# Kernel optimization log

Measured on AMD Instinct MI355X. Metric: run time of the kernel, lower is better.

The kernel has to match this reference:

```python
import jax, jax.numpy as jnp
import numpy as np

EMBED_DIM = 1024
N_HEADS = 16
HEAD_DIM = EMBED_DIM // N_HEADS  # 64
ROPE_DIM = 4
N_FREQ = HEAD_DIM // (2 * ROPE_DIM)  # 8 rotary freqs per coordinate axis
ROPE_THETA = 10000.0
FFN_DIM = 4 * EMBED_DIM
N_TOK = 4096
N_SEQ = 8
EPS = 1e-5
NEG_INF = -1e30


def setup_inputs() -> dict:
    key = jax.random.key(0)
    ks = jax.random.split(key, 16)
    s = 0.02
    coords = jax.random.uniform(ks[0], (N_TOK, ROPE_DIM), jnp.float32) * 10.0
    feats = jax.random.normal(ks[1], (N_TOK, EMBED_DIM), jnp.float32)
    interior = jnp.sort(jax.random.randint(ks[2], (N_SEQ - 1,), 1, N_TOK)).astype(jnp.int32)
    cu_seqlens = jnp.concatenate([jnp.zeros((1,), jnp.int32), interior,
                                  jnp.full((1,), N_TOK, jnp.int32)])
    # learnable RoPE inverse frequencies, one bank per coordinate axis
    base = 1.0 / (ROPE_THETA ** (jnp.arange(N_FREQ, dtype=jnp.float32) * 2.0 * ROPE_DIM / HEAD_DIM))
    inv_freq = jnp.tile(base[None, :], (ROPE_DIM, 1))  # [rope_dim, n_freq]
    return {
        "coords": coords,
        "feats": feats,
        "cu_seqlens": cu_seqlens,
        "Wqkv": jax.random.normal(ks[3], (EMBED_DIM, 3 * EMBED_DIM), jnp.float32) * s,
        "bqkv": jnp.zeros((3 * EMBED_DIM,), jnp.float32),
        "Wo": jax.random.normal(ks[4], (EMBED_DIM, EMBED_DIM), jnp.float32) * s,
        "bo": jnp.zeros((EMBED_DIM,), jnp.float32),
        "inv_freq": inv_freq,
        "ln1_g": jnp.ones((EMBED_DIM,), jnp.float32),
        "ln1_b": jnp.zeros((EMBED_DIM,), jnp.float32),
        "W1": jax.random.normal(ks[5], (EMBED_DIM, FFN_DIM), jnp.float32) * s,
        "b1": jnp.zeros((FFN_DIM,), jnp.float32),
        "W2": jax.random.normal(ks[6], (FFN_DIM, EMBED_DIM), jnp.float32) * s,
        "b2": jnp.zeros((EMBED_DIM,), jnp.float32),
        "ln2_g": jnp.ones((EMBED_DIM,), jnp.float32),
        "ln2_b": jnp.zeros((EMBED_DIM,), jnp.float32),
    }


def _layernorm(x, g, b):
    mu = jnp.mean(x, axis=-1, keepdims=True)
    xc = x - mu
    var = jnp.mean(xc * xc, axis=-1, keepdims=True)
    return xc * jax.lax.rsqrt(var + EPS) * g + b


def _block_forward(coords, feats, cu_seqlens, Wqkv, bqkv, Wo, bo, inv_freq,
                   ln1_g, ln1_b, W1, b1, W2, b2, ln2_g, ln2_b):
    N, D = feats.shape
    qkv = (feats @ Wqkv + bqkv).reshape(N, 3, N_HEADS, HEAD_DIM)
    q, k, v = qkv[:, 0], qkv[:, 1], qkv[:, 2]  # each [N, H, hd]

    # multi-dimensional learnable RoPE: each coord axis rotates its freq bank
    ang = jnp.einsum('nd,df->ndf', coords, inv_freq).reshape(N, 1, HEAD_DIM // 2)
    cos, sin = jnp.cos(ang), jnp.sin(ang)

    def rot(x):
        x1, x2 = jnp.split(x, 2, axis=-1)
        return jnp.concatenate([x1 * cos - x2 * sin, x2 * cos + x1 * sin], axis=-1)

    q, k = rot(q), rot(k)

    # varlen block-diagonal attention mask from cu_seqlens
    seg = jnp.searchsorted(cu_seqlens[1:], jnp.arange(N), side='right')
    mask = seg[:, None] == seg[None, :]  # [N, N]

    scores = jnp.einsum('nhd,mhd->hnm', q, k) / np.sqrt(HEAD_DIM).astype(np.float32)
    scores = jnp.where(mask[None, :, :], scores, NEG_INF)
    attn = jax.nn.softmax(scores, axis=-1)
    o = jnp.einsum('hnm,mhd->nhd', attn, v).reshape(N, D) @ Wo + bo

    h = _layernorm(feats + o, ln1_g, ln1_b)
    f = jax.nn.gelu(h @ W1 + b1) @ W2 + b2
    return _layernorm(h + f, ln2_g, ln2_b)


def reference(coords, feats, cu_seqlens, Wqkv, bqkv, Wo, bo, inv_freq,
              ln1_g, ln1_b, W1, b1, W2, b2, ln2_g, ln2_b):
    return _block_forward(coords, feats, cu_seqlens, Wqkv, bqkv, Wo, bo, inv_freq,
                          ln1_g, ln1_b, W1, b1, W2, b2, ln2_g, ln2_b)
```

## Files before the change

kernel.cpp:

```cpp
#include <hip/hip_runtime.h>

#define NTOK 4096
#define EMB  1024
#define NH   16
#define HD   64
#define FFN  4096

typedef __bf16 bf16x8 __attribute__((ext_vector_type(8)));
typedef float  f32x4  __attribute__((ext_vector_type(4)));

#define ASG __attribute__((address_space(1)))
#define ASL __attribute__((address_space(3)))

__device__ __forceinline__ float b2f(unsigned short u) {
    union { unsigned int i; float f; } v; v.i = ((unsigned int)u) << 16; return v.f;
}
__device__ __forceinline__ unsigned short f2b(float f) {
    union { float f; unsigned int i; } v; v.f = f;
    unsigned int x = v.i;
    return (unsigned short)((x + 0x7fffu + ((x >> 16) & 1u)) >> 16);
}
__device__ __forceinline__ float ldf(const void* p, size_t i, int f32) {
    return f32 ? ((const float*)p)[i] : b2f(((const unsigned short*)p)[i]);
}
__device__ __forceinline__ int probe_f32(const void* p) {
    return ((const unsigned int*)p)[0] == 0x3F800000u ? 1 : 0;
}
__device__ __forceinline__ float gelu_f(float x) {
    float z = 0.7978845608028654f * (x + 0.044715f * x * x * x);
    float t = 1.0f - 2.0f / (__expf(2.0f * z) + 1.0f);
    return 0.5f * x * (1.0f + t);
}
__device__ __forceinline__ void gll16(const void* g, void* l) {
    __builtin_amdgcn_global_load_lds((const ASG void*)g, (ASL void*)l, 16, 0, 0);
}

__global__ __launch_bounds__(256) void convert_kernel(
    const void* __restrict__ feats, const void* __restrict__ bqkv,
    const void* __restrict__ bo, const void* __restrict__ b1,
    const void* __restrict__ b2, const void* __restrict__ g1,
    const void* __restrict__ e1, const void* __restrict__ g2,
    const void* __restrict__ e2, const int* __restrict__ cu,
    unsigned short* __restrict__ feats_bf, unsigned short* __restrict__ smalls,
    int* __restrict__ seg, const void* __restrict__ pr) {
    const int f32 = probe_f32(pr);
    int bid = blockIdx.x, tid = threadIdx.x;
    if (bid < 4096) {
        size_t base = (size_t)bid * 1024 + tid * 4;
        union { unsigned short u[4]; int2 v; } U;
#pragma unroll
        for (int i = 0; i < 4; ++i) U.u[i] = f2b(ldf(feats, base + i, f32));
        *reinterpret_cast<int2*>(&feats_bf[base]) = U.v;
    } else if (bid < 4109) {
        int flat = (bid - 4096) * 1024 + tid * 4;
        const void* src; int off;
        if      (flat < 3072)  { src = bqkv; off = 0; }
        else if (flat < 4096)  { src = bo;   off = 3072; }
        else if (flat < 8192)  { src = b1;   off = 4096; }
        else if (flat < 9216)  { src = b2;   off = 8192; }
        else if (flat < 10240) { src = g1;   off = 9216; }
        else if (flat < 11264) { src = e1;   off = 10240; }
        else if (flat < 12288) { src = g2;   off = 11264; }
        else                   { src = e2;   off = 12288; }
        union { unsigned short u[4]; int2 v; } U;
#pragma unroll
        for (int i = 0; i < 4; ++i) U.u[i] = f2b(ldf(src, flat - off + i, f32));
        *reinterpret_cast<int2*>(&smalls[flat]) = U.v;
    } else {
        int n = (bid - 4109) * 256 + tid;
        int s = 0;
#pragma unroll
        for (int i = 1; i <= 8; ++i) s += (cu[i] <= n) ? 1 : 0;
        seg[n] = s;
    }
}

__global__ __launch_bounds__(256) void transpose_kernel(
    const void* __restrict__ W, unsigned short* __restrict__ O,
    int K, int N, const void* __restrict__ pr) {
    const int f32 = probe_f32(pr);
    int b = blockIdx.x, tid = threadIdx.x;
    int ntiles = N >> 5;
    int nt = b % ntiles, kt = b / ntiles;
    __shared__ unsigned short T[32][33];
    int x = tid & 31, y = tid >> 5;
#pragma unroll
    for (int i = 0; i < 4; ++i) {
        int k = kt * 32 + y + 8 * i, n = nt * 32 + x;
        T[y + 8 * i][x] = f2b(ldf(W, (size_t)k * N + n, f32));
    }
    __syncthreads();
#pragma unroll
    for (int i = 0; i < 4; ++i) {
        int n = nt * 32 + y + 8 * i, k = kt * 32 + x;
        O[(size_t)n * K + k] = T[x][y + 8 * i];
    }
}

template <int ACT, int OUTEXT, int TN>
__global__ __launch_bounds__(256) void gemm128(
    const unsigned short* __restrict__ A, const unsigned short* __restrict__ Bt,
    const unsigned short* __restrict__ bias, void* __restrict__ C,
    int M, int N, int K, int lda, int ldb, const void* __restrict__ pr) {
    constexpr int NB = TN / 32;
    __shared__ __align__(16) unsigned short As[128 * 64];
    __shared__ __align__(16) unsigned short Bs[TN * 64];
    const int f32 = OUTEXT ? probe_f32(pr) : 0;
    const int tid = threadIdx.x;
    const int wave = tid >> 6, lane = tid & 63;
    const int wy = wave >> 1, wx = wave & 1;
    const int qm = lane & 15, quad = lane >> 4;
    const int m0 = blockIdx.y * 128, n0 = blockIdx.x * TN;
    const int r = lane >> 3, gl = lane & 7;

    f32x4 acc[4][NB];
#pragma unroll
    for (int i = 0; i < 4; ++i)
#pragma unroll
        for (int j = 0; j < NB; ++j) acc[i][j] = (f32x4){0.f, 0.f, 0.f, 0.f};

    const unsigned short* Ab = A  + (size_t)m0 * lda;
    const unsigned short* Bb = Bt + (size_t)n0 * ldb;

    for (int k0 = 0; k0 < K; k0 += 64) {
#pragma unroll
        for (int i = 0; i < 4; ++i) {
            int cc = wave * 4 + i;
            gll16(Ab + (size_t)(8 * cc + r) * lda + k0 + ((gl ^ r) << 3), &As[cc * 512]);
        }
#pragma unroll
        for (int i = 0; i < NB; ++i) {
            int cc = wave * NB + i;
            gll16(Bb + (size_t)(8 * cc + r) * ldb + k0 + ((gl ^ r) << 3), &Bs[cc * 512]);
        }
        __syncthreads();
#pragma unroll
        for (int h = 0; h < 2; ++h) {
            bf16x8 af[4], bfr[NB];
#pragma unroll
            for (int i = 0; i < 4; ++i) {
                int phys = (((h * 4 + quad) ^ (qm & 7)) << 3);
                af[i] = *reinterpret_cast<const bf16x8*>(&As[(64 * wy + 16 * i + qm) * 64 + phys]);
            }
#pragma unroll
            for (int j = 0; j < NB; ++j) {
                int phys = (((h * 4 + quad) ^ (qm & 7)) << 3);
                bfr[j] = *reinterpret_cast<const bf16x8*>(&Bs[((TN / 2) * wx + 16 * j + qm) * 64 + phys]);
            }
#pragma unroll
            for (int i = 0; i < 4; ++i)
#pragma unroll
                for (int j = 0; j < NB; ++j)
                    acc[i][j] = __builtin_amdgcn_mfma_f32_16x16x32_bf16(af[i], bfr[j], acc[i][j], 0, 0, 0);
        }
        __syncthreads();
    }
#pragma unroll
    for (int j = 0; j < NB; ++j) {
        int col = n0 + (TN / 2) * wx + 16 * j + qm;
        float bv = b2f(bias[col]);
#pragma unroll
        for (int i = 0; i < 4; ++i) {
            int rowb = m0 + 64 * wy + 16 * i + quad * 4;
#pragma unroll
            for (int rr = 0; rr < 4; ++rr) {
                size_t idx = (size_t)(rowb + rr) * N + col;
                float v = acc[i][j][rr] + bv;
                if (ACT == 1) v = gelu_f(v);
                if (OUTEXT && f32) ((float*)C)[idx] = v;
                else               ((unsigned short*)C)[idx] = f2b(v);
            }
        }
    }
}

__global__ __launch_bounds__(256) void rope_kernel(
    const void* __restrict__ coords, const void* __restrict__ inv_freq,
    unsigned short* __restrict__ qkv, const void* __restrict__ pr) {
    const int f32 = probe_f32(pr);
    int n = blockIdx.x, tid = threadIdx.x;
#pragma unroll
    for (int it = 0; it < 2; ++it) {
        int idx = tid + it * 256;
        int hh = idx >> 5, f = idx & 31;
        float c  = ldf(coords, n * 4 + (f >> 3), f32);
        float iv = ldf(inv_freq, f, f32);
        float sn, cs;
        sincosf(c * iv, &sn, &cs);
#pragma unroll
        for (int w = 0; w < 2; ++w) {
            size_t base = (size_t)n * 3072 + (size_t)w * 1024 + hh * 64;
            float x1 = b2f(qkv[base + f]);
            float x2 = b2f(qkv[base + 32 + f]);
            qkv[base + f]      = f2b(x1 * cs - x2 * sn);
            qkv[base + 32 + f] = f2b(x2 * cs + x1 * sn);
        }
    }
}

__global__ __launch_bounds__(256) void attn_kernel(
    const unsigned short* __restrict__ qkv, const int* __restrict__ seg,
    const int* __restrict__ cu, unsigned short* __restrict__ out) {
    const int h  = blockIdx.y;
    const int t0 = blockIdx.x * 64;
    const int tid  = threadIdx.x;
    const int wave = tid >> 6, lane = tid & 63;
    const int qm = lane & 15, quad = lane >> 4;

    __shared__ __align__(16) unsigned short Ks[64][72];
    __shared__ __align__(16) unsigned short Ps[64][72];
    __shared__ __align__(16) unsigned short Vt[64 * 64];
    __shared__ int segq[64], segk[64];

    const unsigned short* qrow = qkv + (size_t)(t0 + 16 * wave + qm) * 3072 + h * 64;
    bf16x8 af0 = *reinterpret_cast<const bf16x8*>(qrow + quad * 8);
    bf16x8 af1 = *reinterpret_cast<const bf16x8*>(qrow + 32 + quad * 8);

    if (tid < 64) segq[tid] = seg[t0 + tid];
    __syncthreads();

    const int kbeg = cu[segq[0]];
    const int kend = cu[segq[63] + 1];
    int sqr[4];
#pragma unroll
    for (int r = 0; r < 4; ++r) sqr[r] = segq[16 * wave + quad * 4 + r];
    const int wsmin = segq[16 * wave];
    const int wsmax = segq[16 * wave + 15];

    float m[4], l[4];
    f32x4 o[4];
#pragma unroll
    for (int r = 0; r < 4; ++r) { m[r] = -1e30f; l[r] = 0.0f; }
#pragma unroll
    for (int t = 0; t < 4; ++t) o[t] = (f32x4){0.f, 0.f, 0.f, 0.f};

    const int jrow = tid >> 2, dcol = (tid & 3) * 16;
    int4 kA, kB, vA, vB; int sg;
#define LOAD_CHUNK(KC)                                                          \
    {                                                                           \
        int kk = (KC) + jrow;                                                   \
        bool valid = kk < kend;                                                 \
        const unsigned short* kvb = qkv + (size_t)kk * 3072 + h * 64 + dcol;    \
        kA = valid ? *reinterpret_cast<const int4*>(kvb + 1024)     : (int4){0,0,0,0}; \
        kB = valid ? *reinterpret_cast<const int4*>(kvb + 1024 + 8) : (int4){0,0,0,0}; \
        vA = valid ? *reinterpret_cast<const int4*>(kvb + 2048)     : (int4){0,0,0,0}; \
        vB = valid ? *reinterpret_cast<const int4*>(kvb + 2048 + 8) : (int4){0,0,0,0}; \
        sg = 127;                                                               \
        if (tid < 64 && (KC) + tid < kend) sg = seg[(KC) + tid];                \
    }

    LOAD_CHUNK(kbeg);

    for (int kc = kbeg; kc < kend; kc += 64) {
        __syncthreads();
        *reinterpret_cast<int4*>(&Ks[jrow][dcol])     = kA;
        *reinterpret_cast<int4*>(&Ks[jrow][dcol + 8]) = kB;
        {
            union { int4 v; unsigned short u[8]; } U0, U1;
            U0.v = vA; U1.v = vB;
            int g = jrow >> 3, jl = jrow & 7;
#pragma unroll
            for (int i = 0; i < 16; ++i) {
                int d = dcol + i;
                int phys = g ^ (d & 7) ^ ((d >> 3) & 7);
                Vt[d * 64 + phys * 8 + jl] = (i < 8) ? U0.u[i] : U1.u[i - 8];
            }
        }
        if (tid < 64) segk[tid] = sg;
        __syncthreads();

        if (kc + 64 < kend) LOAD_CHUNK(kc + 64);

        const int skmin = segk[0], skmax = segk[63];
        const bool act = !(skmax < wsmin || skmin > wsmax);

        if (act) {
            f32x4 sc[4];
#pragma unroll
            for (int nb = 0; nb < 4; ++nb) {
                bf16x8 bf0 = *reinterpret_cast<const bf16x8*>(&Ks[16 * nb + qm][quad * 8]);
                bf16x8 bf1 = *reinterpret_cast<const bf16x8*>(&Ks[16 * nb + qm][32 + quad * 8]);
                f32x4 s = (f32x4){0.f, 0.f, 0.f, 0.f};
                s = __builtin_amdgcn_mfma_f32_16x16x32_bf16(af0, bf0, s, 0, 0, 0);
                s = __builtin_amdgcn_mfma_f32_16x16x32_bf16(af1, bf1, s, 0, 0, 0);
                sc[nb] = s;
            }
#pragma unroll
            for (int nb = 0; nb < 4; ++nb) {
                int sk = segk[16 * nb + qm];
#pragma unroll
                for (int r = 0; r < 4; ++r)
                    sc[nb][r] = (sk == sqr[r]) ? sc[nb][r] * 0.125f : -1e30f;
            }
            float alpha[4];
#pragma unroll
            for (int r = 0; r < 4; ++r) {
                float v = fmaxf(fmaxf(sc[0][r], sc[1][r]), fmaxf(sc[2][r], sc[3][r]));
                v = fmaxf(v, __shfl_xor(v, 1, 64));
                v = fmaxf(v, __shfl_xor(v, 2, 64));
                v = fmaxf(v, __shfl_xor(v, 4, 64));
                v = fmaxf(v, __shfl_xor(v, 8, 64));
                float mn = fmaxf(m[r], v);
                alpha[r] = __expf(m[r] - mn);
                m[r] = mn;
            }
            float rs[4] = {0.f, 0.f, 0.f, 0.f};
#pragma unroll
            for (int nb = 0; nb < 4; ++nb)
#pragma unroll
                for (int r = 0; r < 4; ++r) {
                    float p = __expf(sc[nb][r] - m[r]);
                    sc[nb][r] = p;
                    rs[r] += p;
                }
#pragma unroll
            for (int r = 0; r < 4; ++r) {
                float v = rs[r];
                v += __shfl_xor(v, 1, 64);
                v += __shfl_xor(v, 2, 64);
                v += __shfl_xor(v, 4, 64);
                v += __shfl_xor(v, 8, 64);
                l[r] = l[r] * alpha[r] + v;
            }
#pragma unroll
            for (int nb = 0; nb < 4; ++nb)
#pragma unroll
                for (int r = 0; r < 4; ++r)
                    Ps[16 * wave + quad * 4 + r][16 * nb + qm] = f2b(sc[nb][r]);
#pragma unroll
            for (int t = 0; t < 4; ++t)
#pragma unroll
                for (int r = 0; r < 4; ++r) o[t][r] *= alpha[r];
        }
        __syncthreads();
        if (act) {
            bf16x8 pa0 = *reinterpret_cast<const bf16x8*>(&Ps[16 * wave + qm][quad * 8]);
            bf16x8 pa1 = *reinterpret_cast<const bf16x8*>(&Ps[16 * wave + qm][32 + quad * 8]);
#pragma unroll
            for (int dt = 0; dt < 4; ++dt) {
                int row = 16 * dt + qm;
                int base = ((row >> 3) & 7) ^ (row & 7);
                bf16x8 vb0 = *reinterpret_cast<const bf16x8*>(&Vt[row * 64 + ((quad ^ base) << 3)]);
                bf16x8 vb1 = *reinterpret_cast<const bf16x8*>(&Vt[row * 64 + (((4 + quad) ^ base) << 3)]);
                o[dt] = __builtin_amdgcn_mfma_f32_16x16x32_bf16(pa0, vb0, o[dt], 0, 0, 0);
                o[dt] = __builtin_amdgcn_mfma_f32_16x16x32_bf16(pa1, vb1, o[dt], 0, 0, 0);
            }
        }
    }
#undef LOAD_CHUNK
    float rl[4];
#pragma unroll
    for (int r = 0; r < 4; ++r) rl[r] = 1.0f / l[r];
#pragma unroll
    for (int dt = 0; dt < 4; ++dt)
#pragma unroll
        for (int r = 0; r < 4; ++r) {
            int row = t0 + 16 * wave + quad * 4 + r;
            out[(size_t)row * 1024 + h * 64 + 16 * dt + qm] = f2b(o[dt][r] * rl[r]);
        }
}

template <int X2EXT, int OUTEXT>
__global__ __launch_bounds__(256) void ln_kernel(
    const unsigned short* __restrict__ x1, const void* __restrict__ x2,
    const unsigned short* __restrict__ g, const unsigned short* __restrict__ b,
    void* __restrict__ out, const void* __restrict__ pr) {
    const int f32 = probe_f32(pr);
    int n = blockIdx.x, tid = threadIdx.x;
    __shared__ float red[8];
    float v[4];
#pragma unroll
    for (int i = 0; i < 4; ++i) {
        int d = tid + i * 256;
        size_t ix = (size_t)n * EMB + d;
        float a2 = (X2EXT && f32) ? ((const float*)x2)[ix]
                                  : b2f(((const unsigned short*)x2)[ix]);
        v[i] = b2f(x1[ix]) + a2;
    }
    float s = v[0] + v[1] + v[2] + v[3];
#pragma unroll
    for (int off = 1; off < 64; off <<= 1) s += __shfl_xor(s, off, 64);
    if ((tid & 63) == 0) red[tid >> 6] = s;
    __syncthreads();
    float mu = (red[0] + red[1] + red[2] + red[3]) * (1.0f / 1024.0f);
    float sq = 0.0f;
#pragma unroll
    for (int i = 0; i < 4; ++i) { float c = v[i] - mu; sq += c * c; }
#pragma unroll
    for (int off = 1; off < 64; off <<= 1) sq += __shfl_xor(sq, off, 64);
    if ((tid & 63) == 0) red[4 + (tid >> 6)] = sq;
    __syncthreads();
    float var = (red[4] + red[5] + red[6] + red[7]) * (1.0f / 1024.0f);
    float rcp = rsqrtf(var + 1e-5f);
#pragma unroll
    for (int i = 0; i < 4; ++i) {
        int d = tid + i * 256;
        size_t ix = (size_t)n * EMB + d;
        float r = (v[i] - mu) * rcp * b2f(g[d]) + b2f(b[d]);
        if (OUTEXT && f32) ((float*)out)[ix] = r;
        else               ((unsigned short*)out)[ix] = f2b(r);
    }
}

extern "C" void kernel_launch(void* const* d_in, const int* in_sizes, int n_in,
                              void* d_out, int out_size, void* d_ws, size_t ws_size,
                              hipStream_t stream) {
    const void* coords   = d_in[0];
    const void* feats    = d_in[1];
    const int*  cu       = (const int*)d_in[2];
    const void* Wqkv     = d_in[3];
    const void* bqkv     = d_in[4];
    const void* Wo       = d_in[5];
    const void* bo       = d_in[6];
    const void* inv_freq = d_in[7];
    const void* ln1_g    = d_in[8];
    const void* ln1_b    = d_in[9];
    const void* W1       = d_in[10];
    const void* b1       = d_in[11];
    const void* W2       = d_in[12];
    const void* b2       = d_in[13];
    const void* ln2_g    = d_in[14];
    const void* ln2_b    = d_in[15];
    const void* pr = ln1_g;

    char* ws = (char*)d_ws;
    int* seg = (int*)ws;
    unsigned short* smalls   = (unsigned short*)(ws + 16384);
    unsigned short* bqkv_bf  = smalls;
    unsigned short* bo_bf    = smalls + 3072;
    unsigned short* b1_bf    = smalls + 4096;
    unsigned short* b2_bf    = smalls + 8192;
    unsigned short* g1_bf    = smalls + 9216;
    unsigned short* e1_bf    = smalls + 10240;
    unsigned short* g2_bf    = smalls + 11264;
    unsigned short* e2_bf    = smalls + 12288;
    unsigned short* feats_bf = (unsigned short*)(ws + 65536);
    unsigned short* hbuf     = feats_bf;
    unsigned short* W1_t     = (unsigned short*)(ws + 8454144);
    unsigned short* Wo_t     = (unsigned short*)(ws + 16842752);
    unsigned short* Wqkv_t   = (unsigned short*)(ws + 18939904);
    unsigned short* qkv      = (unsigned short*)(ws + 25231360);
    unsigned short* attn_o   = (unsigned short*)(ws + 50397184);
    unsigned short* proj     = (unsigned short*)(ws + 25231360);
    unsigned short* W2_t     = (unsigned short*)(ws + 16842752);
    unsigned short* f1       = (unsigned short*)(ws + 25231360);

    hipLaunchKernelGGL(convert_kernel, dim3(4125), dim3(256), 0, stream,
                       feats, bqkv, bo, b1, b2, ln1_g, ln1_b, ln2_g, ln2_b, cu,
                       feats_bf, smalls, seg, pr);
    hipLaunchKernelGGL(transpose_kernel, dim3(3072), dim3(256), 0, stream,
                       Wqkv, Wqkv_t, 1024, 3072, pr);
    hipLaunchKernelGGL(transpose_kernel, dim3(1024), dim3(256), 0, stream,
                       Wo, Wo_t, 1024, 1024, pr);
    hipLaunchKernelGGL(transpose_kernel, dim3(4096), dim3(256), 0, stream,
                       W1, W1_t, 1024, 4096, pr);
    hipLaunchKernelGGL((gemm128<0, 0, 128>), dim3(24, 32), dim3(256), 0, stream,
                       feats_bf, Wqkv_t, bqkv_bf, qkv, NTOK, 3072, 1024, 1024, 1024, pr);
    hipLaunchKernelGGL(rope_kernel, dim3(NTOK), dim3(256), 0, stream,
                       coords, inv_freq, qkv, pr);
    hipLaunchKernelGGL(attn_kernel, dim3(64, NH), dim3(256), 0, stream, qkv, seg, cu, attn_o);
    hipLaunchKernelGGL((gemm128<0, 0, 64>), dim3(16, 32), dim3(256), 0, stream,
                       attn_o, Wo_t, bo_bf, proj, NTOK, 1024, 1024, 1024, 1024, pr);
    hipLaunchKernelGGL(transpose_kernel, dim3(4096), dim3(256), 0, stream,
                       W2, W2_t, 4096, 1024, pr);
    hipLaunchKernelGGL((ln_kernel<0, 0>), dim3(NTOK), dim3(256), 0, stream,
                       feats_bf, proj, g1_bf, e1_bf, hbuf, pr);
    hipLaunchKernelGGL((gemm128<1, 0, 128>), dim3(32, 32), dim3(256), 0, stream,
                       hbuf, W1_t, b1_bf, f1, NTOK, 4096, 1024, 1024, 1024, pr);
    hipLaunchKernelGGL((gemm128<0, 1, 64>), dim3(16, 32), dim3(256), 0, stream,
                       f1, W2_t, b2_bf, d_out, NTOK, 1024, 4096, 4096, 4096, pr);
    hipLaunchKernelGGL((ln_kernel<1, 1>), dim3(NTOK), dim3(256), 0, stream,
                       hbuf, d_out, g2_bf, e2_bf, d_out, pr);
}
```

Measured before the change: 458.6 us.

## Split attention KV range across two blocks, XCD-aware GEMM remap, vectorize layernorm

Attention now splits each query tile's key range into two halves run by separate blocks, which write unnormalized outputs plus per-row max and sum. A new combine kernel merges the two halves with a log-sum-exp rescale. This doubles the attention grid to improve occupancy and balance for long segments. GEMM block indices are remapped so that row panels are grouped per XCD for better L2 reuse, and the layernorm kernel uses vectorized 4-wide loads and stores. Costs are an extra kernel launch, an extra bf16 rounding of the partial outputs, and reuse of the output buffer and workspace as scratch, with the Wo transpose moved later.

```diff
diff --git a/kernel.cpp b/kernel.cpp
--- a/kernel.cpp
+++ b/kernel.cpp
@@ -110,7 +110,16 @@
     const int wave = tid >> 6, lane = tid & 63;
     const int wy = wave >> 1, wx = wave & 1;
     const int qm = lane & 15, quad = lane >> 4;
-    const int m0 = blockIdx.y * 128, n0 = blockIdx.x * TN;
+    int bx, by;
+    if ((gridDim.y & 7) == 0) {
+        int lin = blockIdx.y * gridDim.x + blockIdx.x;
+        int ypg = gridDim.y >> 3;
+        int xcd = lin & 7, s = lin >> 3;
+        int sy = s / gridDim.x;
+        by = xcd * ypg + sy;
+        bx = s - sy * gridDim.x;
+    } else { bx = blockIdx.x; by = blockIdx.y; }
+    const int m0 = by * 128, n0 = bx * TN;
     const int r = lane >> 3, gl = lane & 7;
 
     f32x4 acc[4][NB];
@@ -198,11 +207,13 @@
     }
 }
 
-__global__ __launch_bounds__(256) void attn_kernel(
+__global__ __launch_bounds__(256) void attn_part(
     const unsigned short* __restrict__ qkv, const int* __restrict__ seg,
-    const int* __restrict__ cu, unsigned short* __restrict__ out) {
+    const int* __restrict__ cu, unsigned short* __restrict__ u0,
+    unsigned short* __restrict__ u1, float* __restrict__ ml) {
     const int h  = blockIdx.y;
-    const int t0 = blockIdx.x * 64;
+    const int piece = blockIdx.x & 1;
+    const int t0 = (blockIdx.x >> 1) * 64;
     const int tid  = threadIdx.x;
     const int wave = tid >> 6, lane = tid & 63;
     const int qm = lane & 15, quad = lane >> 4;
@@ -219,8 +230,13 @@
     if (tid < 64) segq[tid] = seg[t0 + tid];
     __syncthreads();
 
-    const int kbeg = cu[segq[0]];
-    const int kend = cu[segq[63] + 1];
+    const int kbegT = cu[segq[0]];
+    const int kendT = cu[segq[63] + 1];
+    const int nchunks = (kendT - kbegT + 63) >> 6;
+    const int half = (nchunks + 1) >> 1;
+    const int kb = kbegT + (piece ? half * 64 : 0);
+    const int ke = piece ? kendT : min(kendT, kbegT + half * 64);
+
     int sqr[4];
 #pragma unroll
     for (int r = 0; r < 4; ++r) sqr[r] = segq[16 * wave + quad * 4 + r];
@@ -239,19 +255,19 @@
 #define LOAD_CHUNK(KC)                                                          \
     {                                                                           \
         int kk = (KC) + jrow;                                                   \
-        bool valid = kk < kend;                                                 \
+        bool valid = kk < ke;                                                   \
         const unsigned short* kvb = qkv + (size_t)kk * 3072 + h * 64 + dcol;    \
         kA = valid ? *reinterpret_cast<const int4*>(kvb + 1024)     : (int4){0,0,0,0}; \
         kB = valid ? *reinterpret_cast<const int4*>(kvb + 1024 + 8) : (int4){0,0,0,0}; \
         vA = valid ? *reinterpret_cast<const int4*>(kvb + 2048)     : (int4){0,0,0,0}; \
         vB = valid ? *reinterpret_cast<const int4*>(kvb + 2048 + 8) : (int4){0,0,0,0}; \
         sg = 127;                                                               \
-        if (tid < 64 && (KC) + tid < kend) sg = seg[(KC) + tid];                \
-    }
-
-    LOAD_CHUNK(kbeg);
-
-    for (int kc = kbeg; kc < kend; kc += 64) {
+        if (tid < 64 && (KC) + tid < ke) sg = seg[(KC) + tid];                  \
+    }
+
+    if (kb < ke) LOAD_CHUNK(kb);
+
+    for (int kc = kb; kc < ke; kc += 64) {
         __syncthreads();
         *reinterpret_cast<int4*>(&Ks[jrow][dcol])     = kA;
         *reinterpret_cast<int4*>(&Ks[jrow][dcol + 8]) = kB;
@@ -269,7 +285,7 @@
         if (tid < 64) segk[tid] = sg;
         __syncthreads();
 
-        if (kc + 64 < kend) LOAD_CHUNK(kc + 64);
+        if (kc + 64 < ke) LOAD_CHUNK(kc + 64);
 
         const int skmin = segk[0], skmax = segk[63];
         const bool act = !(skmax < wsmin || skmin > wsmax);
@@ -348,16 +364,43 @@
         }
     }
 #undef LOAD_CHUNK
-    float rl[4];
-#pragma unroll
-    for (int r = 0; r < 4; ++r) rl[r] = 1.0f / l[r];
+    unsigned short* dst = piece ? u1 : u0;
 #pragma unroll
     for (int dt = 0; dt < 4; ++dt)
 #pragma unroll
         for (int r = 0; r < 4; ++r) {
             int row = t0 + 16 * wave + quad * 4 + r;
-            out[(size_t)row * 1024 + h * 64 + 16 * dt + qm] = f2b(o[dt][r] * rl[r]);
-        }
+            dst[(size_t)row * 1024 + h * 64 + 16 * dt + qm] = f2b(o[dt][r]);
+        }
+    if (qm == 0) {
+        float2* ML = (float2*)ml;
+#pragma unroll
+        for (int r = 0; r < 4; ++r) {
+            int row = t0 + 16 * wave + quad * 4 + r;
+            ML[((piece * 16 + h) << 12) + row] = make_float2(m[r], l[r]);
+        }
+    }
+}
+
+__global__ __launch_bounds__(256) void combine_kernel(
+    const unsigned short* __restrict__ u1, const float* __restrict__ ml,
+    unsigned short* __restrict__ u0out) {
+    int n = blockIdx.x, tid = threadIdx.x;
+    int d4 = tid * 4, h = tid >> 4;
+    const float2* ML = (const float2*)ml;
+    float2 p0 = ML[(h << 12) + n];
+    float2 p1 = ML[((16 + h) << 12) + n];
+    float M = fmaxf(p0.x, p1.x);
+    float a0 = __expf(p0.x - M), a1 = __expf(p1.x - M);
+    float rcp = 1.0f / (a0 * p0.y + a1 * p1.y);
+    size_t ix = (size_t)n * 1024 + d4;
+    union { int2 q; unsigned short u[4]; } A, B, R;
+    A.q = *reinterpret_cast<const int2*>(u0out + ix);
+    B.q = *reinterpret_cast<const int2*>(u1 + ix);
+#pragma unroll
+    for (int i = 0; i < 4; ++i)
+        R.u[i] = f2b((a0 * b2f(A.u[i]) + a1 * b2f(B.u[i])) * rcp);
+    *reinterpret_cast<int2*>(u0out + ix) = R.q;
 }
 
 template <int X2EXT, int OUTEXT>
@@ -368,14 +411,22 @@
     const int f32 = probe_f32(pr);
     int n = blockIdx.x, tid = threadIdx.x;
     __shared__ float red[8];
+    const int d0 = tid * 4;
+    const size_t ix0 = (size_t)n * EMB + d0;
     float v[4];
-#pragma unroll
-    for (int i = 0; i < 4; ++i) {
-        int d = tid + i * 256;
-        size_t ix = (size_t)n * EMB + d;
-        float a2 = (X2EXT && f32) ? ((const float*)x2)[ix]
-                                  : b2f(((const unsigned short*)x2)[ix]);
-        v[i] = b2f(x1[ix]) + a2;
+    {
+        union { int2 q; unsigned short u[4]; } A;
+        A.q = *reinterpret_cast<const int2*>(&x1[ix0]);
+        if (X2EXT && f32) {
+            float4 B = *reinterpret_cast<const float4*>((const float*)x2 + ix0);
+            v[0] = b2f(A.u[0]) + B.x; v[1] = b2f(A.u[1]) + B.y;
+            v[2] = b2f(A.u[2]) + B.z; v[3] = b2f(A.u[3]) + B.w;
+        } else {
+            union { int2 q; unsigned short u[4]; } B;
+            B.q = *reinterpret_cast<const int2*>((const unsigned short*)x2 + ix0);
+#pragma unroll
+            for (int i = 0; i < 4; ++i) v[i] = b2f(A.u[i]) + b2f(B.u[i]);
+        }
     }
     float s = v[0] + v[1] + v[2] + v[3];
 #pragma unroll
@@ -392,13 +443,22 @@
     __syncthreads();
     float var = (red[4] + red[5] + red[6] + red[7]) * (1.0f / 1024.0f);
     float rcp = rsqrtf(var + 1e-5f);
-#pragma unroll
-    for (int i = 0; i < 4; ++i) {
-        int d = tid + i * 256;
-        size_t ix = (size_t)n * EMB + d;
-        float r = (v[i] - mu) * rcp * b2f(g[d]) + b2f(b[d]);
-        if (OUTEXT && f32) ((float*)out)[ix] = r;
-        else               ((unsigned short*)out)[ix] = f2b(r);
+    union { int2 q; unsigned short u[4]; } G, Bb;
+    G.q  = *reinterpret_cast<const int2*>(&g[d0]);
+    Bb.q = *reinterpret_cast<const int2*>(&b[d0]);
+    if (OUTEXT && f32) {
+        float4 R;
+        R.x = (v[0] - mu) * rcp * b2f(G.u[0]) + b2f(Bb.u[0]);
+        R.y = (v[1] - mu) * rcp * b2f(G.u[1]) + b2f(Bb.u[1]);
+        R.z = (v[2] - mu) * rcp * b2f(G.u[2]) + b2f(Bb.u[2]);
+        R.w = (v[3] - mu) * rcp * b2f(G.u[3]) + b2f(Bb.u[3]);
+        *reinterpret_cast<float4*>((float*)out + ix0) = R;
+    } else {
+        union { int2 q; unsigned short u[4]; } R;
+#pragma unroll
+        for (int i = 0; i < 4; ++i)
+            R.u[i] = f2b((v[i] - mu) * rcp * b2f(G.u[i]) + b2f(Bb.u[i]));
+        *reinterpret_cast<int2*>((unsigned short*)out + ix0) = R.q;
     }
 }
 
@@ -437,28 +497,33 @@
     unsigned short* feats_bf = (unsigned short*)(ws + 65536);
     unsigned short* hbuf     = feats_bf;
     unsigned short* W1_t     = (unsigned short*)(ws + 8454144);
-    unsigned short* Wo_t     = (unsigned short*)(ws + 16842752);
+    unsigned short* u1buf    = (unsigned short*)(ws + 16842752);
     unsigned short* Wqkv_t   = (unsigned short*)(ws + 18939904);
     unsigned short* qkv      = (unsigned short*)(ws + 25231360);
     unsigned short* attn_o   = (unsigned short*)(ws + 50397184);
+    unsigned short* Wo_t     = (unsigned short*)(ws + 18939904);
+    unsigned short* W2_t     = (unsigned short*)(ws + 16842752);
     unsigned short* proj     = (unsigned short*)(ws + 25231360);
-    unsigned short* W2_t     = (unsigned short*)(ws + 16842752);
     unsigned short* f1       = (unsigned short*)(ws + 25231360);
+    float* mlbuf = (float*)d_out;
 
     hipLaunchKernelGGL(convert_kernel, dim3(4125), dim3(256), 0, stream,
                        feats, bqkv, bo, b1, b2, ln1_g, ln1_b, ln2_g, ln2_b, cu,
                        feats_bf, smalls, seg, pr);
     hipLaunchKernelGGL(transpose_kernel, dim3(3072), dim3(256), 0, stream,
                        Wqkv, Wqkv_t, 1024, 3072, pr);
-    hipLaunchKernelGGL(transpose_kernel, dim3(1024), dim3(256), 0, stream,
-                       Wo, Wo_t, 1024, 1024, pr);
     hipLaunchKernelGGL(transpose_kernel, dim3(4096), dim3(256), 0, stream,
                        W1, W1_t, 1024, 4096, pr);
     hipLaunchKernelGGL((gemm128<0, 0, 128>), dim3(24, 32), dim3(256), 0, stream,
                        feats_bf, Wqkv_t, bqkv_bf, qkv, NTOK, 3072, 1024, 1024, 1024, pr);
     hipLaunchKernelGGL(rope_kernel, dim3(NTOK), dim3(256), 0, stream,
                        coords, inv_freq, qkv, pr);
-    hipLaunchKernelGGL(attn_kernel, dim3(64, NH), dim3(256), 0, stream, qkv, seg, cu, attn_o);
+    hipLaunchKernelGGL(attn_part, dim3(128, NH), dim3(256), 0, stream,
+                       qkv, seg, cu, attn_o, u1buf, mlbuf);
+    hipLaunchKernelGGL(combine_kernel, dim3(NTOK), dim3(256), 0, stream,
+                       u1buf, mlbuf, attn_o);
+    hipLaunchKernelGGL(transpose_kernel, dim3(1024), dim3(256), 0, stream,
+                       Wo, Wo_t, 1024, 1024, pr);
     hipLaunchKernelGGL((gemm128<0, 0, 64>), dim3(16, 32), dim3(256), 0, stream,
                        attn_o, Wo_t, bo_bf, proj, NTOK, 1024, 1024, 1024, 1024, pr);
     hipLaunchKernelGGL(transpose_kernel, dim3(4096), dim3(256), 0, stream,
```

Measured after the change: 448.9 us. -2.1%, faster.
